# Optimization experiments

Measured on AMD Instinct MI355X. Metric: run time of the kernel, lower is better.

Reference implementation:

```python
import jax, jax.numpy as jnp
import numpy as np

L, D, H, V, BS = 12, 768, 12, 50257, 1024  # n_layer, n_embd, n_head, vocab, block_size
B, T = 2, 1024
HD = D // H
SCALE = HD ** -0.5


def setup_inputs() -> dict:
    key = jax.random.key(0)
    ks = jax.random.split(key, 10)
    s = 0.02  # init std from _init_weights
    f = lambda k, shape: jax.random.normal(k, shape, jnp.float32) * s
    return {
        "idx": jax.random.randint(ks[0], (B, T), 0, V),
        "tok_emb": f(ks[1], (V, D)),          # tied with LM head
        "pos_emb": f(ks[2], (BS, D)),
        "wqkv": f(ks[3], (L, 3 * D, D)), "bqkv": jnp.zeros((L, 3 * D), jnp.float32),
        "wproj": f(ks[4], (L, D, D)),    "bproj": jnp.zeros((L, D), jnp.float32),
        "ln1_g": jnp.ones((L, D), jnp.float32), "ln1_b": jnp.zeros((L, D), jnp.float32),
        "ln2_g": jnp.ones((L, D), jnp.float32), "ln2_b": jnp.zeros((L, D), jnp.float32),
        "w1": f(ks[5], (L, 4 * D, D)), "b1": jnp.zeros((L, 4 * D), jnp.float32),
        "w2": f(ks[6], (L, D, 4 * D)), "b2": jnp.zeros((L, D), jnp.float32),
        "lnf_g": jnp.ones((D,), jnp.float32), "lnf_b": jnp.zeros((D,), jnp.float32),
    }


def _ln(x, g, b, eps=1e-5):
    mu = jnp.mean(x, axis=-1, keepdims=True)
    var = jnp.mean(jnp.square(x - mu), axis=-1, keepdims=True)
    return (x - mu) * jax.lax.rsqrt(var + eps) * g + b


def _gpt_forward(idx, tok_emb, pos_emb, wqkv, bqkv, wproj, bproj,
                 ln1_g, ln1_b, ln2_g, ln2_b, w1, b1, w2, b2, lnf_g, lnf_b):
    Bb, Tt = idx.shape
    x = tok_emb[idx] + pos_emb[:Tt]  # [B,T,D]; dropout=0 in eval
    causal = jnp.tril(jnp.ones((Tt, Tt), bool))

    def block(x, p):
        wq, bq, wp, bp, g1, be1, g2, be2, W1, B1, W2, B2 = p
        h = _ln(x, g1, be1)
        qkv = h @ wq.T + bq                       # [B,T,3D]
        q, k, v = jnp.split(qkv, 3, axis=-1)
        to_heads = lambda z: z.reshape(Bb, Tt, H, HD).transpose(0, 2, 1, 3)
        q, k, v = to_heads(q), to_heads(k), to_heads(v)
        att = jnp.einsum('bhqd,bhkd->bhqk', q, k) * SCALE
        att = jnp.where(causal, att, -jnp.inf)
        att = jax.nn.softmax(att, axis=-1)
        y = jnp.einsum('bhqk,bhkd->bhqd', att, v)
        y = y.transpose(0, 2, 1, 3).reshape(Bb, Tt, D)
        x = x + (y @ wp.T + bp)
        h2 = _ln(x, g2, be2)
        ff = jax.nn.gelu(h2 @ W1.T + B1, approximate=False) @ W2.T + B2
        return x + ff, None

    layer_params = (wqkv, bqkv, wproj, bproj, ln1_g, ln1_b, ln2_g, ln2_b, w1, b1, w2, b2)
    x, _ = jax.lax.scan(block, x, layer_params)
    x = _ln(x, lnf_g, lnf_b)
    return x @ tok_emb.T  # tied LM head, [B,T,V]


def reference(idx, tok_emb, pos_emb, wqkv, bqkv, wproj, bproj,
              ln1_g, ln1_b, ln2_g, ln2_b, w1, b1, w2, b2, lnf_g, lnf_b):
    return _gpt_forward(idx, tok_emb, pos_emb, wqkv, bqkv, wproj, bproj,
                        ln1_g, ln1_b, ln2_g, ln2_b, w1, b1, w2, b2, lnf_g, lnf_b)
```

## Files before the change

kernel.cpp:

```cpp
#include <hip/hip_runtime.h>
#include <hip/hip_bf16.h>
#include <type_traits>

#define TT 1024
#define DD 768
#define HH 12
#define LL 12
#define VV 50257
#define MROWS 2048

typedef __attribute__((ext_vector_type(4))) float f32x4;
typedef __attribute__((ext_vector_type(16))) float f32x16;
typedef __attribute__((ext_vector_type(8))) short bf16x8;

__device__ __forceinline__ short f2bf(float f) {
  __hip_bfloat16 h = __float2bfloat16(f);
  short s;
  __builtin_memcpy(&s, &h, 2);
  return s;
}

__device__ __forceinline__ void gload16(const void* g, void* l) {
  __builtin_amdgcn_global_load_lds(
      (const __attribute__((address_space(1))) unsigned int*)g,
      (__attribute__((address_space(3))) unsigned int*)l, 16, 0, 0);
}

__device__ __forceinline__ float wsum(float v) {
#pragma unroll
  for (int o = 32; o; o >>= 1) v += __shfl_xor(v, o, 64);
  return v;
}

struct CvtArgs { const float* s[5]; short* d[5]; long n4[5]; };

__global__ __launch_bounds__(256) void cvt5_k(CvtArgs a, long tot)
{
  const long stride = (long)gridDim.x * 256;
  for (long i = (long)blockIdx.x * 256 + threadIdx.x; i < tot; i += stride) {
    long off = i;
    int s = 0;
#pragma unroll
    for (int q = 0; q < 4; ++q) {
      if (off >= a.n4[s]) { off -= a.n4[s]; ++s; }
    }
    const float4 v = ((const float4*)a.s[s])[off];
    short4 h;
    h.x = f2bf(v.x); h.y = f2bf(v.y); h.z = f2bf(v.z); h.w = f2bf(v.w);
    ((short4*)a.d[s])[off] = h;
  }
}

__global__ __launch_bounds__(256) void embed_k(const int* __restrict__ idx,
    const float* __restrict__ tok, const float* __restrict__ pos,
    float* __restrict__ x)
{
  int i = blockIdx.x * 256 + threadIdx.x;
  int d = i % DD;
  int bt = i / DD;
  int t = bt & (TT - 1);
  x[i] = tok[(long)idx[bt] * DD + d] + pos[t * DD + d];
}

__global__ __launch_bounds__(256) void ln_k(const float* __restrict__ x,
    const float* __restrict__ g, const float* __restrict__ b,
    short* __restrict__ out)
{
  const int w = threadIdx.x >> 6;
  const int lane = threadIdx.x & 63;
  const int row = blockIdx.x * 4 + w;
  const float* xr = x + (long)row * DD;
  float4 v[3];
  float s = 0.f, s2 = 0.f;
#pragma unroll
  for (int i = 0; i < 3; ++i) {
    v[i] = ((const float4*)xr)[lane + i * 64];
    s  += v[i].x + v[i].y + v[i].z + v[i].w;
    s2 += v[i].x * v[i].x + v[i].y * v[i].y + v[i].z * v[i].z + v[i].w * v[i].w;
  }
  s = wsum(s); s2 = wsum(s2);
  const float mu = s * (1.f / DD);
  const float var = s2 * (1.f / DD) - mu * mu;
  const float rstd = rsqrtf(var + 1e-5f);
#pragma unroll
  for (int i = 0; i < 3; ++i) {
    const int d0 = (lane + i * 64) * 4;
    short4 h;
    h.x = f2bf((v[i].x - mu) * rstd * g[d0 + 0] + b[d0 + 0]);
    h.y = f2bf((v[i].y - mu) * rstd * g[d0 + 1] + b[d0 + 1]);
    h.z = f2bf((v[i].z - mu) * rstd * g[d0 + 2] + b[d0 + 2]);
    h.w = f2bf((v[i].w - mu) * rstd * g[d0 + 3] + b[d0 + 3]);
    ((short4*)(out + (long)row * DD))[lane + i * 64] = h;
  }
}

__global__ __launch_bounds__(256) void flash_k(const short* __restrict__ qkv,
                                               const short* __restrict__ vt,
                                               short* __restrict__ y)
{
  const int qt = (int)gridDim.x - 1 - (int)blockIdx.x;
  const int z  = blockIdx.y;
  const int zb = z / HH, zh = z % HH;
  const int w    = threadIdx.x >> 6;
  const int lane = threadIdx.x & 63;
  const int c = lane & 15, g = lane >> 4;

  __shared__ __align__(16) short Pl[4][16][72];
  __shared__ float Ol[4][16][64];
  __shared__ float ml[4][16], ll[4][16];

  const int qbase = qt * 16;
  const long rowQ = (long)(zb * TT + qbase + c) * (3 * DD) + zh * 64;

  bf16x8 qf[2];
  qf[0] = *(const bf16x8*)(qkv + rowQ + g * 8);
  qf[1] = *(const bf16x8*)(qkv + rowQ + 32 + g * 8);

  f32x4 O[4] = {};
  f32x4 mrun, lrun;
#pragma unroll
  for (int r = 0; r < 4; ++r) { mrun[r] = -1e30f; lrun[r] = 0.f; }

  const float CSC = 0.125f * 1.44269504089f;
  const int nt = (qbase + 15) / 64 + 1;

  for (int t = w; t < nt; t += 4) {
    const int k0 = t * 64;
    f32x4 acc[4] = {};
#pragma unroll
    for (int nf = 0; nf < 4; ++nf) {
      const long rowK = (long)(zb * TT + k0 + nf * 16 + c) * (3 * DD) + DD + zh * 64;
      bf16x8 kf0 = *(const bf16x8*)(qkv + rowK + g * 8);
      bf16x8 kf1 = *(const bf16x8*)(qkv + rowK + 32 + g * 8);
      acc[nf] = __builtin_amdgcn_mfma_f32_16x16x32_bf16(qf[0], kf0, acc[nf], 0, 0, 0);
      acc[nf] = __builtin_amdgcn_mfma_f32_16x16x32_bf16(qf[1], kf1, acc[nf], 0, 0, 0);
    }
    f32x4 tv[4];
    const int mask_needed = (k0 + 63 > qbase);
#pragma unroll
    for (int nf = 0; nf < 4; ++nf) {
      const int k_abs = k0 + nf * 16 + c;
#pragma unroll
      for (int r = 0; r < 4; ++r) {
        float val = acc[nf][r] * CSC;
        if (mask_needed && k_abs > qbase + g * 4 + r) val = -1e30f;
        tv[nf][r] = val;
      }
    }
    f32x4 rmax;
#pragma unroll
    for (int r = 0; r < 4; ++r)
      rmax[r] = fmaxf(fmaxf(tv[0][r], tv[1][r]), fmaxf(tv[2][r], tv[3][r]));
#pragma unroll
    for (int off = 1; off < 16; off <<= 1) {
#pragma unroll
      for (int r = 0; r < 4; ++r) rmax[r] = fmaxf(rmax[r], __shfl_xor(rmax[r], off, 64));
    }
    f32x4 mnew, rfac;
#pragma unroll
    for (int r = 0; r < 4; ++r) {
      mnew[r] = fmaxf(mrun[r], rmax[r]);
      rfac[r] = exp2f(mrun[r] - mnew[r]);
      mrun[r] = mnew[r];
    }
    f32x4 e[4], rsum;
#pragma unroll
    for (int r = 0; r < 4; ++r) rsum[r] = 0.f;
#pragma unroll
    for (int nf = 0; nf < 4; ++nf)
#pragma unroll
      for (int r = 0; r < 4; ++r) {
        e[nf][r] = exp2f(tv[nf][r] - mnew[r]);
        rsum[r] += e[nf][r];
      }
#pragma unroll
    for (int off = 1; off < 16; off <<= 1) {
#pragma unroll
      for (int r = 0; r < 4; ++r) rsum[r] += __shfl_xor(rsum[r], off, 64);
    }
#pragma unroll
    for (int r = 0; r < 4; ++r) lrun[r] = lrun[r] * rfac[r] + rsum[r];
#pragma unroll
    for (int nf = 0; nf < 4; ++nf)
#pragma unroll
      for (int r = 0; r < 4; ++r) O[nf][r] *= rfac[r];
#pragma unroll
    for (int nf = 0; nf < 4; ++nf)
#pragma unroll
      for (int r = 0; r < 4; ++r)
        Pl[w][g * 4 + r][nf * 16 + c] = f2bf(e[nf][r]);
    asm volatile("s_waitcnt lgkmcnt(0)" ::: "memory");
    bf16x8 pf[2];
    pf[0] = *(const bf16x8*)&Pl[w][c][g * 8];
    pf[1] = *(const bf16x8*)&Pl[w][c][32 + g * 8];
#pragma unroll
    for (int nf = 0; nf < 4; ++nf) {
      const long vrow = ((long)z * 64 + nf * 16 + c) * TT + k0;
      const bf16x8 vf0 = *(const bf16x8*)(vt + vrow + g * 8);
      const bf16x8 vf1 = *(const bf16x8*)(vt + vrow + 32 + g * 8);
      O[nf] = __builtin_amdgcn_mfma_f32_16x16x32_bf16(pf[0], vf0, O[nf], 0, 0, 0);
      O[nf] = __builtin_amdgcn_mfma_f32_16x16x32_bf16(pf[1], vf1, O[nf], 0, 0, 0);
    }
  }

#pragma unroll
  for (int nf = 0; nf < 4; ++nf)
#pragma unroll
    for (int r = 0; r < 4; ++r)
      Ol[w][g * 4 + r][nf * 16 + c] = O[nf][r];
  if (c == 0) {
#pragma unroll
    for (int r = 0; r < 4; ++r) { ml[w][g * 4 + r] = mrun[r]; ll[w][g * 4 + r] = lrun[r]; }
  }
  __syncthreads();

  for (int e2 = threadIdx.x; e2 < 16 * 64; e2 += 256) {
    const int row = e2 >> 6, d = e2 & 63;
    const float M = fmaxf(fmaxf(ml[0][row], ml[1][row]), fmaxf(ml[2][row], ml[3][row]));
    float L = 0.f, Ov = 0.f;
#pragma unroll
    for (int u = 0; u < 4; ++u) {
      const float f = exp2f(ml[u][row] - M);
      L += ll[u][row] * f;
      Ov += Ol[u][row][d] * f;
    }
    y[(long)(zb * TT + qbase + row) * DD + zh * 64 + d] = f2bf(Ov / L);
  }
}

template<int BM, int BN, int BK, int MFS, typename TB, int EPI, bool LMSWZ, bool PIPE>
__global__ __launch_bounds__(256) void gemm_nt(
    const short* __restrict__ A, const TB* __restrict__ Bm,
    const float* __restrict__ bias, const float* __restrict__ resid,
    void* __restrict__ Cout,
    int M, int N, int K, int lda, int ldb, int ldc,
    long aSB, long aSH, long bSB, long bSH, long cSB, long cSH,
    float scale, int causal)
{
  int n0, m0;
  if constexpr (LMSWZ) {
    const int l = blockIdx.x;
    const int x = l & 7;
    const int j = l >> 3;
    const int mt = j & 15;
    const int nl = j >> 4;
    const int npan = (N + BN - 1) / BN;
    const int q = npan >> 3, rr = npan & 7;
    const int cnt = q + (x < rr);
    if (nl >= cnt) return;
    const int nstart = x * q + (x < rr ? x : rr);
    n0 = (nstart + nl) * BN;
    m0 = mt * BM;
  } else {
    n0 = blockIdx.x * BN;
    m0 = blockIdx.y * BM;
  }
  if (causal && n0 >= m0 + BM) return;
  const int z = blockIdx.z;
  const int zb = z / HH, zh = z % HH;
  const short* Ag = A + zb * aSB + zh * aSH + (long)m0 * lda;
  const TB*    Bg = Bm + zb * bSB + zh * bSH;
  const long  cOff = zb * cSB + zh * cSH;

  constexpr int NBUF = PIPE ? 2 : 1;
  static_assert(MFS == 16 || (BM == BN && !PIPE), "ILV path needs BM==BN, single-buffer");
  __shared__ __align__(16) short LDSb[NBUF * (BM + BN) * BK];

  const int tid = threadIdx.x;
  const int lane = tid & 63, wid = tid >> 6;
  constexpr int WTM = BM / 2, WTN = BN / 2;
  constexpr int FM = WTM / 16, FN = WTN / 16;
  constexpr int FM2 = (MFS == 32) ? WTM / 32 : 1;
  constexpr int FN2 = (MFS == 32) ? WTN / 32 : 1;
  constexpr int AM = (MFS == 16) ? FM : FM2;
  constexpr int AN = (MFS == 16) ? FN : FN2;
  const int wr = wid >> 1, wc = wid & 1;

  using accT = typename std::conditional<MFS == 16, f32x4, f32x16>::type;
  accT acc[AM][AN] = {};

  constexpr bool B_IS_F32 = (sizeof(TB) == 4);
  constexpr int CPR = BK / 8;
  constexpr int NCA = BM * CPR;
  constexpr int NCB = BN * CPR;
  constexpr int IA = NCA / 256, IB = NCB / 256;
  constexpr int GPT = IA + IB;
  static_assert(CPR == 8, "swizzle assumes 128B operand rows (BK=64)");
  static_assert(B_IS_F32 || (NCA % 256 == 0 && NCB % 256 == 0), "chunk grid");

  auto aTile = [&](int buf) -> short* { return LDSb + buf * BM * BK; };
  auto bTile = [&](int buf) -> short* { return LDSb + NBUF * BM * BK + buf * BN * BK; };

  auto compute = [&](int buf) {
    if constexpr (MFS == 16) {
      const int kAoff = (lane >> 4) * 8;
      short* Als = aTile(buf);
      short* Bls = bTile(buf);
#pragma unroll
      for (int kk = 0; kk < BK; kk += 32) {
        bf16x8 af[AM], bfr[AN];
#pragma unroll
        for (int mi = 0; mi < AM; ++mi) {
          const int Ra = wr * WTM + mi * 16 + (lane & 15);
          const int kca = (kk + kAoff) >> 3;
          af[mi] = *(const bf16x8*)&Als[Ra * BK + ((kca ^ (Ra & 7)) << 3)];
        }
#pragma unroll
        for (int ni = 0; ni < AN; ++ni) {
          const int Rb = wc * WTN + ni * 16 + (lane & 15);
          const int kcb = (kk + kAoff) >> 3;
          bfr[ni] = *(const bf16x8*)&Bls[Rb * BK + ((kcb ^ (Rb & 7)) << 3)];
        }
#pragma unroll
        for (int mi = 0; mi < AM; ++mi)
#pragma unroll
          for (int ni = 0; ni < AN; ++ni)
            acc[mi][ni] = __builtin_amdgcn_mfma_f32_16x16x32_bf16(af[mi], bfr[ni], acc[mi][ni], 0, 0, 0);
      }
    } else {
#pragma unroll
      for (int kk = 0; kk < BK; kk += 16) {
        const int kc = (kk >> 3) + (lane >> 5);
        bf16x8 af[AM], bfr[AN];
#pragma unroll
        for (int mi = 0; mi < AM; ++mi) {
          const int Ra = wr * WTM + mi * 32 + (lane & 31);
          af[mi] = *(const bf16x8*)&LDSb[Ra * (2 * BK) + ((kc ^ (Ra & 15)) << 3)];
        }
#pragma unroll
        for (int ni = 0; ni < AN; ++ni) {
          const int Rb = wc * WTN + ni * 32 + (lane & 31);
          bfr[ni] = *(const bf16x8*)&LDSb[Rb * (2 * BK) + (((8 + kc) ^ (Rb & 15)) << 3)];
        }
#pragma unroll
        for (int mi = 0; mi < AM; ++mi)
#pragma unroll
          for (int ni = 0; ni < AN; ++ni)
            acc[mi][ni] = __builtin_amdgcn_mfma_f32_32x32x16_bf16(af[mi], bfr[ni], acc[mi][ni], 0, 0, 0);
      }
    }
  };

  if constexpr (!B_IS_F32) {
    const int ldsoff = wid * 64 * 16;
    if constexpr (MFS == 32) {
      constexpr int IT = BM * 16 / 256;
      const short* abp[IT];
#pragma unroll
      for (int i = 0; i < IT; ++i) {
        const int cc = i * 256 + tid;
        const int r = cc >> 4, cl = cc & 15;
        const int co = cl ^ (r & 15);
        if (co < 8) {
          abp[i] = Ag + (long)r * lda + co * 8;
        } else {
          int gr = n0 + r; gr = (gr < N) ? gr : (N - 1);
          abp[i] = (const short*)Bg + (long)gr * ldb + (co - 8) * 8;
        }
      }
      const int KT = K / BK;
      for (int kt = 0; kt < KT; ++kt) {
#pragma unroll
        for (int i = 0; i < IT; ++i) {
          gload16(abp[i], (char*)LDSb + i * 4096 + ldsoff);
          abp[i] += BK;
        }
        __syncthreads();
        compute(0);
        __syncthreads();
      }
    } else {
      const short* ap[IA];
      const short* bp[IB];
#pragma unroll
      for (int i = 0; i < IA; ++i) {
        const int cch = i * 256 + tid;
        const int r = cch / CPR, kc = cch % CPR;
        ap[i] = Ag + (long)r * lda + ((kc ^ (r & 7)) << 3);
      }
#pragma unroll
      for (int i = 0; i < IB; ++i) {
        const int cch = i * 256 + tid;
        const int r = cch / CPR, kc = cch % CPR;
        int gr = n0 + r; gr = (gr < N) ? gr : (N - 1);
        bp[i] = (const short*)Bg + (long)gr * ldb + ((kc ^ (r & 7)) << 3);
      }

      auto stage = [&](int buf) {
#pragma unroll
        for (int i = 0; i < IA; ++i) {
          gload16(ap[i], (char*)aTile(buf) + i * 4096 + ldsoff);
          ap[i] += BK;
        }
#pragma unroll
        for (int i = 0; i < IB; ++i) {
          gload16(bp[i], (char*)bTile(buf) + i * 4096 + ldsoff);
          bp[i] += BK;
        }
      };

      if constexpr (PIPE) {
        const int KT = K / BK;
        stage(0);
        for (int kt = 0; kt < KT; ++kt) {
          const int cur = kt & 1;
          if (kt + 1 < KT) {
            stage(cur ^ 1);
            asm volatile("s_waitcnt vmcnt(%0)" :: "i"(GPT));
          } else {
            asm volatile("s_waitcnt vmcnt(0)");
          }
          __builtin_amdgcn_sched_barrier(0);
          __builtin_amdgcn_s_barrier();
          __builtin_amdgcn_sched_barrier(0);
          compute(cur);
          asm volatile("" ::: "memory");
          __builtin_amdgcn_s_barrier();
          __builtin_amdgcn_sched_barrier(0);
        }
      } else {
        const int KT = K / BK;
        for (int kt = 0; kt < KT; ++kt) {
          stage(0);
          __syncthreads();
          compute(0);
          __syncthreads();
        }
      }
    }
  } else {
    for (int k0 = 0; k0 < K; k0 += BK) {
      if constexpr (MFS == 32) {
#pragma unroll
        for (int cc = tid; cc < BM * CPR; cc += 256) {
          int r = cc / CPR, kc = cc % CPR;
          const uint4 v = *(const uint4*)(Ag + (long)r * lda + k0 + kc * 8);
          *(uint4*)&LDSb[r * (2 * BK) + ((kc ^ (r & 15)) << 3)] = v;
        }
#pragma unroll
        for (int cc = tid; cc < BN * (BK / 4); cc += 256) {
          int r = cc / (BK / 4), kc4 = cc % (BK / 4);
          int gr = n0 + r; gr = (gr < N) ? gr : (N - 1);
          const float4 v = *(const float4*)((const float*)Bg + (long)gr * ldb + k0 + kc4 * 4);
          short4 h4;
          h4.x = f2bf(v.x); h4.y = f2bf(v.y); h4.z = f2bf(v.z); h4.w = f2bf(v.w);
          const int co = 8 + (kc4 >> 1);
          *(short4*)&LDSb[r * (2 * BK) + ((co ^ (r & 15)) << 3) + (kc4 & 1) * 4] = h4;
        }
      } else {
        short* Als = aTile(0);
        short* Bls = bTile(0);
#pragma unroll
        for (int cc = tid; cc < BM * CPR; cc += 256) {
          int r = cc / CPR, kc = cc % CPR;
          const uint4 v = *(const uint4*)(Ag + (long)r * lda + k0 + kc * 8);
          *(uint4*)&Als[r * BK + ((kc ^ (r & 7)) << 3)] = v;
        }
#pragma unroll
        for (int cc = tid; cc < BN * (BK / 4); cc += 256) {
          int r = cc / (BK / 4), kc4 = cc % (BK / 4);
          int gr = n0 + r; gr = (gr < N) ? gr : (N - 1);
          const float4 v = *(const float4*)((const float*)Bg + (long)gr * ldb + k0 + kc4 * 4);
          short4 h4;
          h4.x = f2bf(v.x); h4.y = f2bf(v.y); h4.z = f2bf(v.z); h4.w = f2bf(v.w);
          const int co = kc4 >> 1;
          *(short4*)&Bls[r * BK + ((co ^ (r & 7)) << 3) + (kc4 & 1) * 4] = h4;
        }
      }
      __syncthreads();
      compute(0);
      __syncthreads();
    }
  }

  if constexpr (MFS == 16) {
    const int rq = (lane >> 4) << 2;
    const int cl = lane & 15;
#pragma unroll
    for (int mi = 0; mi < AM; ++mi) {
#pragma unroll
      for (int ni = 0; ni < AN; ++ni) {
        const int cg = n0 + wc * WTN + ni * 16 + cl;
        if (cg >= N) continue;
        const int rbase = m0 + wr * WTM + mi * 16 + rq;
        if constexpr (EPI == 5) {
          if (cg >= 2 * DD) {
            const int hh = (cg - 2 * DD) >> 6, dd2 = (cg - 2 * DD) & 63;
            const int bI = rbase >> 10, tI = rbase & (TT - 1);
            const float bv = bias[cg];
            short4 h4;
            h4.x = f2bf(acc[mi][ni][0] + bv);
            h4.y = f2bf(acc[mi][ni][1] + bv);
            h4.z = f2bf(acc[mi][ni][2] + bv);
            h4.w = f2bf(acc[mi][ni][3] + bv);
            short* vtp = (short*)(void*)resid;
            *(short4*)(vtp + (((long)(bI * HH + hh) * 64 + dd2) << 10) + tI) = h4;
          } else {
#pragma unroll
            for (int q = 0; q < 4; ++q)
              ((short*)Cout)[(long)(rbase + q) * ldc + cg] = f2bf(acc[mi][ni][q] + bias[cg]);
          }
          continue;
        }
#pragma unroll
        for (int q = 0; q < 4; ++q) {
          const long cidx = cOff + (long)(rbase + q) * ldc + cg;
          const float v = acc[mi][ni][q];
          if constexpr (EPI == 0) {
            ((float*)Cout)[cidx] = v * scale;
          } else if constexpr (EPI == 1) {
            ((short*)Cout)[cidx] = f2bf(v + bias[cg]);
          } else if constexpr (EPI == 2) {
            ((float*)Cout)[cidx] = resid[cidx] + v + bias[cg];
          } else if constexpr (EPI == 3) {
            const float zz = v + bias[cg];
            ((short*)Cout)[cidx] = f2bf(0.5f * zz * (1.f + erff(zz * 0.70710678118f)));
          } else {
            ((short*)Cout)[cidx] = f2bf(v);
          }
        }
      }
    }
  } else {
    const int cl = lane & 31;
    const int rhi = (lane >> 5) * 4;
#pragma unroll
    for (int mi = 0; mi < AM; ++mi) {
#pragma unroll
      for (int ni = 0; ni < AN; ++ni) {
        const int cg = n0 + wc * WTN + ni * 32 + cl;
        if (cg >= N) continue;
#pragma unroll
        for (int reg = 0; reg < 16; ++reg) {
          const int row = m0 + wr * WTM + mi * 32 + (reg & 3) + ((reg >> 2) * 8) + rhi;
          const long cidx = cOff + (long)row * ldc + cg;
          const float v = acc[mi][ni][reg];
          if constexpr (EPI == 0) {
            ((float*)Cout)[cidx] = v * scale;
          } else if constexpr (EPI == 1) {
            ((short*)Cout)[cidx] = f2bf(v + bias[cg]);
          } else if constexpr (EPI == 2) {
            ((float*)Cout)[cidx] = resid[cidx] + v + bias[cg];
          } else if constexpr (EPI == 3) {
            const float zz = v + bias[cg];
            ((short*)Cout)[cidx] = f2bf(0.5f * zz * (1.f + erff(zz * 0.70710678118f)));
          } else {
            ((short*)Cout)[cidx] = f2bf(v);
          }
        }
      }
    }
  }
}

template<typename TB>
static void run_model(const int* idx, const float* tok_f, const float* pos,
                      const TB* wqkv, const float* bqkv, const TB* wproj, const float* bproj,
                      const float* ln1g, const float* ln1b, const float* ln2g, const float* ln2b,
                      const TB* w1, const float* b1, const TB* w2, const float* b2,
                      const float* lnfg, const float* lnfb, const TB* tok_w,
                      float* xa, float* xb, short* hbf, short* qkv, short* vt,
                      short* ybf, short* ffb,
                      float* out, hipStream_t stream)
{
  embed_k<<<dim3(MROWS * DD / 256), 256, 0, stream>>>(idx, tok_f, pos, xa);

  float* xc = xa;
  float* xn = xb;
  for (int l = 0; l < LL; ++l) {
    ln_k<<<dim3(MROWS / 4), 256, 0, stream>>>(xc, ln1g + l * DD, ln1b + l * DD, hbf);
    gemm_nt<128, 64, 64, 16, TB, 5, false, true><<<dim3(36, 16, 1), 256, 0, stream>>>(
        hbf, wqkv + (long)l * 3 * DD * DD, bqkv + l * 3 * DD, (const float*)vt, qkv,
        MROWS, 3 * DD, DD, DD, DD, 3 * DD, 0, 0, 0, 0, 0, 0, 1.f, 0);
    flash_k<<<dim3(64, 24), 256, 0, stream>>>(qkv, vt, ybf);
    gemm_nt<64, 64, 64, 16, TB, 2, false, true><<<dim3(12, 32, 1), 256, 0, stream>>>(
        ybf, wproj + (long)l * DD * DD, bproj + l * DD, xc, xn,
        MROWS, DD, DD, DD, DD, DD, 0, 0, 0, 0, 0, 0, 1.f, 0);
    ln_k<<<dim3(MROWS / 4), 256, 0, stream>>>(xn, ln2g + l * DD, ln2b + l * DD, hbf);
    gemm_nt<128, 64, 64, 16, TB, 3, false, true><<<dim3(48, 16, 1), 256, 0, stream>>>(
        hbf, w1 + (long)l * 4 * DD * DD, b1 + l * 4 * DD, nullptr, ffb,
        MROWS, 4 * DD, DD, DD, DD, 4 * DD, 0, 0, 0, 0, 0, 0, 1.f, 0);
    gemm_nt<64, 64, 64, 16, TB, 2, false, true><<<dim3(12, 32, 1), 256, 0, stream>>>(
        ffb, w2 + (long)l * DD * 4 * DD, b2 + l * DD, xn, xc,
        MROWS, DD, 4 * DD, 4 * DD, 4 * DD, DD, 0, 0, 0, 0, 0, 0, 1.f, 0);
  }
  ln_k<<<dim3(MROWS / 4), 256, 0, stream>>>(xc, lnfg, lnfb, hbf);
  gemm_nt<128, 128, 64, 32, TB, 0, true, false><<<dim3(6400, 1, 1), 256, 0, stream>>>(
      hbf, tok_w, nullptr, nullptr, out,
      MROWS, VV, DD, DD, DD, VV, 0, 0, 0, 0, 0, 0, 1.f, 0);
}

extern "C" void kernel_launch(void* const* d_in, const int* in_sizes, int n_in,
                              void* d_out, int out_size, void* d_ws, size_t ws_size,
                              hipStream_t stream)
{
  const int*   idx  = (const int*)d_in[0];
  const float* tok  = (const float*)d_in[1];
  const float* pos  = (const float*)d_in[2];
  const float* wqkv = (const float*)d_in[3];
  const float* bqkv = (const float*)d_in[4];
  const float* wproj= (const float*)d_in[5];
  const float* bproj= (const float*)d_in[6];
  const float* ln1g = (const float*)d_in[7];
  const float* ln1b = (const float*)d_in[8];
  const float* ln2g = (const float*)d_in[9];
  const float* ln2b = (const float*)d_in[10];
  const float* w1   = (const float*)d_in[11];
  const float* b1   = (const float*)d_in[12];
  const float* w2   = (const float*)d_in[13];
  const float* b2   = (const float*)d_in[14];
  const float* lnfg = (const float*)d_in[15];
  const float* lnfb = (const float*)d_in[16];
  float* out = (float*)d_out;

  const long E_WQKV = (long)LL * 3 * DD * DD;
  const long E_WPRJ = (long)LL * DD * DD;
  const long E_W1   = (long)LL * 4 * DD * DD;
  const long E_W2   = E_W1;
  const long E_TOK  = (long)VV * DD;
  const long E_WSUM = E_WQKV + E_WPRJ + E_W1 + E_W2 + E_TOK;

  const size_t NEED_B = 44040192;
  const size_t NEED_A = NEED_B + 2 * (size_t)E_WSUM;

  if (ws_size < NEED_B) return;
  const bool bf16w = (ws_size >= NEED_A);

  char* ws = (char*)d_ws;
  short *wqkv_h = nullptr, *wprj_h = nullptr, *w1_h = nullptr, *w2_h = nullptr, *tok_h = nullptr;
  if (bf16w) {
    wqkv_h = (short*)ws; ws += E_WQKV * 2;
    wprj_h = (short*)ws; ws += E_WPRJ * 2;
    w1_h   = (short*)ws; ws += E_W1 * 2;
    w2_h   = (short*)ws; ws += E_W2 * 2;
    tok_h  = (short*)ws; ws += E_TOK * 2;
  }
  float* xa  = (float*)ws; ws += (size_t)MROWS * DD * 4;
  float* xb  = (float*)ws; ws += (size_t)MROWS * DD * 4;
  short* hbf = (short*)ws; ws += (size_t)MROWS * DD * 2;
  short* qkv = (short*)ws; ws += (size_t)MROWS * 3 * DD * 2;
  short* vt  = (short*)ws; ws += (size_t)24 * 64 * TT * 2;
  short* ybf = (short*)ws; ws += (size_t)MROWS * DD * 2;
  short* ffb = (short*)ws; ws += (size_t)MROWS * 4 * DD * 2;

  if (bf16w) {
    CvtArgs ca;
    ca.s[0] = wqkv; ca.d[0] = wqkv_h; ca.n4[0] = E_WQKV / 4;
    ca.s[1] = wproj; ca.d[1] = wprj_h; ca.n4[1] = E_WPRJ / 4;
    ca.s[2] = w1;   ca.d[2] = w1_h;   ca.n4[2] = E_W1 / 4;
    ca.s[3] = w2;   ca.d[3] = w2_h;   ca.n4[3] = E_W2 / 4;
    ca.s[4] = tok;  ca.d[4] = tok_h;  ca.n4[4] = E_TOK / 4;
    const long tot = (E_WQKV + E_WPRJ + E_W1 + E_W2 + E_TOK) / 4;
    cvt5_k<<<dim3(4096), 256, 0, stream>>>(ca, tot);
    run_model<short>(idx, tok, pos, wqkv_h, bqkv, wprj_h, bproj,
                     ln1g, ln1b, ln2g, ln2b, w1_h, b1, w2_h, b2, lnfg, lnfb, tok_h,
                     xa, xb, hbf, qkv, vt, ybf, ffb, out, stream);
  } else {
    run_model<float>(idx, tok, pos, wqkv, bqkv, wproj, bproj,
                     ln1g, ln1b, ln2g, ln2b, w1, b1, w2, b2, lnfg, lnfb, tok,
                     xa, xb, hbf, qkv, vt, ybf, ffb, out, stream);
  }
}
```

Baseline: 2.019 ms.

## Add dedicated 256x256 double-buffered LM-head GEMM kernel with 512 threads

Adds a specialised LM-head GEMM that uses 256x256 output tiles, 8 waves, and double-buffered LDS staging through direct global-to-LDS loads with a partial vmcnt wait. It replaces the previous single-buffered 128x128 MFMA32 path for the vocab projection whenever the weight type is bf16, and drops that older MFS==32 branch. Larger tiles cut repeated global reads of A and B for the largest GEMM, and the double buffering overlaps loads with MFMA work. In exchange it uses about 128KB of LDS and 128 accumulator floats per thread, which limits occupancy.

Result: no change. 2.030 ms (+0.6%).

```diff
diff --git a/kernel.cpp b/kernel.cpp
--- a/kernel.cpp
+++ b/kernel.cpp
@@ -225,6 +225,114 @@
       Ov += Ol[u][row][d] * f;
     }
     y[(long)(zb * TT + qbase + row) * DD + zh * 64 + d] = f2bf(Ov / L);
+  }
+}
+
+__global__ __launch_bounds__(512) void gemm_lm(
+    const short* __restrict__ A, const short* __restrict__ Bm,
+    float* __restrict__ C, int M, int N, int K, int lda, int ldb, int ldc)
+{
+  const int l = blockIdx.x;
+  const int x = l & 7;
+  const int j = l >> 3;
+  const int mt = j & 7;
+  const int nl = j >> 3;
+  const int npan = (N + 255) / 256;
+  const int q = npan >> 3, rr = npan & 7;
+  const int cnt = q + (x < rr);
+  if (nl >= cnt) return;
+  const int nstart = x * q + (x < rr ? x : rr);
+  const int n0 = (nstart + nl) * 256;
+  const int m0 = mt * 256;
+
+  __shared__ __align__(16) short Als[2][256][64];
+  __shared__ __align__(16) short Bls[2][256][64];
+
+  const int tid = threadIdx.x;
+  const int lane = tid & 63, wid = tid >> 6;
+  const int wr = wid >> 2, wc = wid & 3;
+
+  f32x4 acc[8][4] = {};
+  const int kAoff = (lane >> 4) * 8;
+
+  const short* ap[4];
+  const short* bp[4];
+#pragma unroll
+  for (int i = 0; i < 4; ++i) {
+    const int cc = i * 512 + tid;
+    const int r = cc >> 3, kc = cc & 7;
+    ap[i] = A + (long)(m0 + r) * lda + ((kc ^ (r & 7)) << 3);
+    int gr = n0 + r; gr = (gr < N) ? gr : (N - 1);
+    bp[i] = Bm + (long)gr * ldb + ((kc ^ (r & 7)) << 3);
+  }
+  const int ldsoff = wid * 64 * 16;
+
+  auto stage = [&](int buf) {
+#pragma unroll
+    for (int i = 0; i < 4; ++i) {
+      gload16(ap[i], (char*)&Als[buf][0][0] + i * 8192 + ldsoff);
+      ap[i] += 64;
+    }
+#pragma unroll
+    for (int i = 0; i < 4; ++i) {
+      gload16(bp[i], (char*)&Bls[buf][0][0] + i * 8192 + ldsoff);
+      bp[i] += 64;
+    }
+  };
+
+  auto compute = [&](int buf) {
+#pragma unroll
+    for (int kk = 0; kk < 64; kk += 32) {
+      const int kc = (kk + kAoff) >> 3;
+      bf16x8 bfr[4];
+#pragma unroll
+      for (int ni = 0; ni < 4; ++ni) {
+        const int Rb = wc * 64 + ni * 16 + (lane & 15);
+        bfr[ni] = *(const bf16x8*)&Bls[buf][Rb][(kc ^ (Rb & 7)) << 3];
+      }
+#pragma unroll
+      for (int mi = 0; mi < 8; ++mi) {
+        const int Ra = wr * 128 + mi * 16 + (lane & 15);
+        const bf16x8 af = *(const bf16x8*)&Als[buf][Ra][(kc ^ (Ra & 7)) << 3];
+#pragma unroll
+        for (int ni = 0; ni < 4; ++ni)
+          acc[mi][ni] = __builtin_amdgcn_mfma_f32_16x16x32_bf16(af, bfr[ni], acc[mi][ni], 0, 0, 0);
+      }
+    }
+  };
+
+  const int KT = K / 64;
+  stage(0);
+  for (int kt = 0; kt < KT; ++kt) {
+    const int cur = kt & 1;
+    if (kt + 1 < KT) {
+      stage(cur ^ 1);
+      asm volatile("s_waitcnt vmcnt(8)");
+    } else {
+      asm volatile("s_waitcnt vmcnt(0)");
+    }
+    __builtin_amdgcn_sched_barrier(0);
+    __builtin_amdgcn_s_barrier();
+    __builtin_amdgcn_sched_barrier(0);
+    compute(cur);
+    asm volatile("" ::: "memory");
+    __builtin_amdgcn_s_barrier();
+    __builtin_amdgcn_sched_barrier(0);
+  }
+
+  const int rq = (lane >> 4) << 2;
+  const int cl = lane & 15;
+#pragma unroll
+  for (int mi = 0; mi < 8; ++mi) {
+#pragma unroll
+    for (int ni = 0; ni < 4; ++ni) {
+      const int cg = n0 + wc * 64 + ni * 16 + cl;
+      if (cg >= N) continue;
+      const int rbase = m0 + wr * 128 + mi * 16 + rq;
+#pragma unroll
+      for (int qq = 0; qq < 4; ++qq)
+        C[(long)(rbase + qq) * ldc + cg] = acc[mi][ni][qq];
+    }
   }
 }
 
@@ -343,33 +451,7 @@
 
   if constexpr (!B_IS_F32) {
     const int ldsoff = wid * 64 * 16;
-    if constexpr (MFS == 32) {
-      constexpr int IT = BM * 16 / 256;
-      const short* abp[IT];
-#pragma unroll
-      for (int i = 0; i < IT; ++i) {
-        const int cc = i * 256 + tid;
-        const int r = cc >> 4, cl = cc & 15;
-        const int co = cl ^ (r & 15);
-        if (co < 8) {
-          abp[i] = Ag + (long)r * lda + co * 8;
-        } else {
-          int gr = n0 + r; gr = (gr < N) ? gr : (N - 1);
-          abp[i] = (const short*)Bg + (long)gr * ldb + (co - 8) * 8;
-        }
-      }
-      const int KT = K / BK;
-      for (int kt = 0; kt < KT; ++kt) {
-#pragma unroll
-        for (int i = 0; i < IT; ++i) {
-          gload16(abp[i], (char*)LDSb + i * 4096 + ldsoff);
-          abp[i] += BK;
-        }
-        __syncthreads();
-        compute(0);
-        __syncthreads();
-      }
-    } else {
+    {
       const short* ap[IA];
       const short* bp[IB];
 #pragma unroll
@@ -585,9 +667,14 @@
         MROWS, DD, 4 * DD, 4 * DD, 4 * DD, DD, 0, 0, 0, 0, 0, 0, 1.f, 0);
   }
   ln_k<<<dim3(MROWS / 4), 256, 0, stream>>>(xc, lnfg, lnfb, hbf);
-  gemm_nt<128, 128, 64, 32, TB, 0, true, false><<<dim3(6400, 1, 1), 256, 0, stream>>>(
-      hbf, tok_w, nullptr, nullptr, out,
-      MROWS, VV, DD, DD, DD, VV, 0, 0, 0, 0, 0, 0, 1.f, 0);
+  if constexpr (sizeof(TB) == 2) {
+    gemm_lm<<<dim3(1600, 1, 1), 512, 0, stream>>>(
+        hbf, (const short*)tok_w, out, MROWS, VV, DD, DD, DD, VV);
+  } else {
+    gemm_nt<128, 128, 64, 32, TB, 0, true, false><<<dim3(6400, 1, 1), 256, 0, stream>>>(
+        hbf, tok_w, nullptr, nullptr, out,
+        MROWS, VV, DD, DD, DD, VV, 0, 0, 0, 0, 0, 0, 1.f, 0);
+  }
 }
 
 extern "C" void kernel_launch(void* const* d_in, const int* in_sizes, int n_in,
```
